# Kernel optimization log

Hardware: AMD Instinct MI355X
Metric: run time of the kernel (lower is better)

Reference implementation:

```python
import jax, jax.numpy as jnp
import numpy as np
from jax import lax

K = 64            # top-k channels kept per spatial location
GAMMA = 1.0       # noise scale (forward default)
NOISE_SCALE = 8.0 / 255.0


def setup_inputs() -> dict:
    key = jax.random.key(0)
    k1, k2, k3, k4 = jax.random.split(key, 4)
    B, Cin, Cout, H, W = 32, 128, 256, 64, 64
    x = jax.random.normal(k1, (B, Cin, H, W), dtype=jnp.float32)
    weight = jax.random.normal(k2, (Cout, Cin, 3, 3), dtype=jnp.float32) * 0.05
    relu_bias = jax.random.normal(k3, (Cout,), dtype=jnp.float32) * 0.1
    noise_u = jax.random.uniform(k4, (B, Cout, H, W), dtype=jnp.float32)
    return {"x": x, "weight": weight, "relu_bias": relu_bias, "noise_u": noise_u}


def reference(x, weight, relu_bias, noise_u):
    # conv3x3, stride 1, SAME padding, no bias (NCHW / OIHW)
    o = lax.conv_general_dilated(
        x, weight, window_strides=(1, 1), padding="SAME",
        dimension_numbers=("NCHW", "OIHW", "NCHW"))

    # per-output-channel bias = sum |W| over (in, kh, kw)  -> (1, Cout, 1, 1)
    bias = jnp.sum(jnp.abs(weight), axis=(1, 2, 3)).reshape(1, -1, 1, 1)

    # training-time uniform noise in [-gamma, gamma) scaled by bias*8/255
    o = o + bias * NOISE_SCALE * (noise_u * (2.0 * GAMMA) - GAMMA)

    # top-k masking over the channel dimension (per pixel)
    oc = jnp.moveaxis(o, 1, -1)                 # (B, H, W, C)
    topvals, _ = lax.top_k(oc, K)               # (B, H, W, K)
    thresh = topvals[..., K - 1:K]              # kth largest
    oc = jnp.where(oc >= thresh, oc, 0.0)
    o = jnp.moveaxis(oc, -1, 1)                 # back to (B, C, H, W)

    # trainable-bias ReLU: relu(o + b_c)
    o = jnp.maximum(o + relu_bias.reshape(1, -1, 1, 1), 0.0)
    return o
```

## Files before the change

kernel.cpp:

```cpp
#include <hip/hip_runtime.h>
#include <stdint.h>

#define BB 32
#define CIN 128
#define COUT 256
#define HH 64
#define WW 64
#define TOPK 64
#define NS_F (8.0f/255.0f)
#define GAPF 5e-4f
#define NS_D (8.0/255.0)
#define EPI_STRIDE 258
#define LIST_CAP 65536
#define XT_BYTES 33792

typedef __bf16 bf16x8 __attribute__((ext_vector_type(8)));
typedef float f32x4 __attribute__((ext_vector_type(4)));

__device__ __forceinline__ unsigned short bf_bits(float v) {
    __bf16 b = (__bf16)v;
    return __builtin_bit_cast(unsigned short, b);
}
__device__ __forceinline__ float bf_round(float v) { return (float)(__bf16)v; }

__device__ __forceinline__ int xoff(int ww, int s, int ci) {
    int byte = (ww << 9) + (s << 8) + (ci << 1);
    return byte ^ ((ww & 7) << 4);
}

__device__ __forceinline__ uint32_t skey32(float v) {
    uint32_t b = __float_as_uint(v);
    return (b & 0x80000000u) ? ~b : (b | 0x80000000u);
}
__device__ __forceinline__ float unskey32(uint32_t k) {
    uint32_t b = (k & 0x80000000u) ? (k & 0x7FFFFFFFu) : ~k;
    return __uint_as_float(b);
}

__device__ __forceinline__ uint64_t sortkey(double v) {
    uint64_t b = (uint64_t)__double_as_longlong(v);
    return (b & 0x8000000000000000ULL) ? ~b : (b | 0x8000000000000000ULL);
}
__device__ __forceinline__ double unsortkey(uint64_t k) {
    uint64_t b = (k & 0x8000000000000000ULL) ? (k & 0x7FFFFFFFFFFFFFFFULL) : ~k;
    return __longlong_as_double((long long)b);
}

__device__ __forceinline__ void select64_u32(const uint32_t u[4], uint32_t& k64, uint32_t& k65, int& bestcnt) {
    uint32_t prefix = 0;
    bestcnt = 256;
    for (int bit = 31; bit >= 0; --bit) {
        uint32_t cand = prefix | (1u << bit);
        int cnt = __popcll(__ballot(u[0] >= cand)) + __popcll(__ballot(u[1] >= cand))
                + __popcll(__ballot(u[2] >= cand)) + __popcll(__ballot(u[3] >= cand));
        if (cnt >= TOPK) {
            prefix = cand;
            bestcnt = cnt;
            if (cnt == TOPK) break;
        }
    }
    uint32_t mn = 0xFFFFFFFFu, mx = 0u;
#pragma unroll
    for (int j = 0; j < 4; ++j) {
        if (u[j] >= prefix) { if (u[j] < mn) mn = u[j]; }
        else                { if (u[j] > mx) mx = u[j]; }
    }
    for (int m = 1; m < 64; m <<= 1) {
        uint32_t a = (uint32_t)__shfl_xor((int)mn, m, 64);
        if (a < mn) mn = a;
        uint32_t b = (uint32_t)__shfl_xor((int)mx, m, 64);
        if (b > mx) mx = b;
    }
    k64 = mn; k65 = mx;
}

__device__ __forceinline__ void select64(const uint64_t u[4], uint64_t& k64, uint64_t& k65) {
    uint64_t prefix = 0;
    for (int bit = 63; bit >= 0; --bit) {
        uint64_t cand = prefix | (1ULL << bit);
        int cnt = __popcll(__ballot(u[0] >= cand)) + __popcll(__ballot(u[1] >= cand))
                + __popcll(__ballot(u[2] >= cand)) + __popcll(__ballot(u[3] >= cand));
        if (cnt >= TOPK) {
            prefix = cand;
            if (cnt == TOPK) break;
        }
    }
    uint64_t mn = ~0ULL, mx = 0ULL;
#pragma unroll
    for (int j = 0; j < 4; ++j) {
        if (u[j] >= prefix) { if (u[j] < mn) mn = u[j]; }
        else                { if (u[j] > mx) mx = u[j]; }
    }
    for (int m = 1; m < 64; m <<= 1) {
        uint64_t a = (uint64_t)__shfl_xor((unsigned long long)mn, m, 64);
        if (a < mn) mn = a;
        uint64_t b = (uint64_t)__shfl_xor((unsigned long long)mx, m, 64);
        if (b > mx) mx = b;
    }
    k64 = mn; k65 = mx;
}

__global__ __launch_bounds__(256) void prep_absw(const float* __restrict__ w,
                                                 double* __restrict__ absw,
                                                 int* __restrict__ counter) {
    const int c = blockIdx.x;
    const int t = threadIdx.x;
    if (c == 0 && t == 0) counter[0] = 0;
    double s = 0.0;
    for (int k = t; k < CIN * 9; k += 256) s += fabs((double)w[c * (CIN * 9) + k]);
    __shared__ double red[4];
    for (int m = 32; m; m >>= 1) s += __shfl_xor(s, m, 64);
    if ((t & 63) == 0) red[t >> 6] = s;
    __syncthreads();
    if (t == 0) absw[c] = red[0] + red[1] + red[2] + red[3];
}

__global__ __launch_bounds__(256) void prep_wT(const float* __restrict__ w,
                                               float* __restrict__ wT) {
    const int o0 = blockIdx.x * 16;
    const int c = threadIdx.x;
#pragma unroll
    for (int i = 0; i < 16; ++i) {
        int o = o0 + i;
        int r = o >> 7, ci = o & 127;
        wT[(size_t)o * COUT + c] = w[(size_t)(c * CIN + ci) * 9 + r];
    }
}

__global__ __launch_bounds__(128) void prep_wB(const float* __restrict__ w,
                                               unsigned short* __restrict__ wB) {
    const int c = blockIdx.x;
    const int ci = threadIdx.x;
#pragma unroll
    for (int r = 0; r < 9; ++r) {
        float v = w[((size_t)c * CIN + ci) * 9 + r];
        float hf = bf_round(v);
        wB[((size_t)r * COUT + c) * CIN + ci] = bf_bits(v);
        wB[((size_t)(9 + r) * COUT + c) * CIN + ci] = bf_bits(v - hf);
    }
}

__global__ __launch_bounds__(256, 2) void fused_kernel(
    const float* __restrict__ x,
    const float* __restrict__ relu_bias,
    const float* __restrict__ noise,
    const double* __restrict__ absw,
    const unsigned short* __restrict__ wB,
    float* __restrict__ out,
    int* __restrict__ counter,
    int* __restrict__ list) {

    __shared__ alignas(16) union {
        unsigned short xT[2 * 66 * 256];
        float o[32 * EPI_STRIDE];
    } U;
    __shared__ float lds_absw[COUT];
    __shared__ float lds_bias[COUT];
    __shared__ uint32_t thrk[32];

    const int tid = threadIdx.x;
    const int lane = tid & 63;
    const int wv = tid >> 6;

    const int bid = ((int)(blockIdx.x & 7) << 7) + ((int)blockIdx.x >> 3);
    const int b0 = (bid >> 6) * 2;
    const int h = bid & 63;

    lds_absw[tid] = (float)absw[tid];
    lds_bias[tid] = relu_bias[tid];

    const int kgrp8 = (lane >> 4) << 3;

    f32x4 acc[2][4][4];
#pragma unroll
    for (int g = 0; g < 2; ++g)
#pragma unroll
        for (int i = 0; i < 4; ++i)
#pragma unroll
            for (int j = 0; j < 4; ++j) {
                acc[g][i][j][0] = 0.f; acc[g][i][j][1] = 0.f;
                acc[g][i][j][2] = 0.f; acc[g][i][j][3] = 0.f;
            }

    char* xb = (char*)U.xT;

    if (tid < 128) {
        int img = tid >> 6;
        int t = tid & 63;
        int wwz = (t & 32) ? 65 : 0;
        int sz = (t >> 4) & 1;
        int c0z = (t & 15) << 3;
        bf16x8 z;
#pragma unroll
        for (int j = 0; j < 8; ++j) z[j] = (__bf16)0.f;
        *(bf16x8*)(xb + img * XT_BYTES + xoff(wwz, sz, c0z)) = z;
    }

    const int laneB = ((lane & 15) << 7) + ((lane >> 4) << 3) + (wv << 13);

    for (int kh = 0; kh < 3; ++kh) {
        const int r = h + kh - 1;
        if (r < 0 || r >= HH) continue;
        __syncthreads();
        {
            const int w = lane;
#pragma unroll
            for (int img = 0; img < 2; ++img) {
                const float* xr = x + (((size_t)(b0 + img) * CIN) * HH + (size_t)r) * WW;
                char* xbi = xb + img * XT_BYTES;
#pragma unroll
                for (int rep = 0; rep < 4; ++rep) {
                    const int c0 = rep * 32 + wv * 8;
                    const float* px = xr + (size_t)c0 * (HH * WW) + w;
                    bf16x8 hv, lv;
#pragma unroll
                    for (int j = 0; j < 8; ++j) {
                        float v = px[j * (HH * WW)];
                        float hf = bf_round(v);
                        hv[j] = (__bf16)v;
                        lv[j] = (__bf16)(v - hf);
                    }
                    *(bf16x8*)(xbi + xoff(w + 1, 0, c0)) = hv;
                    *(bf16x8*)(xbi + xoff(w + 1, 1, c0)) = lv;
                }
            }
        }
        __syncthreads();
#pragma unroll 1
        for (int ci0 = 0; ci0 < CIN; ci0 += 32) {
#pragma unroll
            for (int kw = 0; kw < 3; ++kw) {
                const unsigned short* wp0 = wB + (size_t)(kh * 3 + kw) * 32768 + ci0 + laneB;
                const unsigned short* wp1 = wp0 + (size_t)9 * 32768;
                bf16x8 bh[4], bl[4];
#pragma unroll
                for (int nt = 0; nt < 4; ++nt) {
                    bh[nt] = *(const bf16x8*)(wp0 + nt * 2048);
                    bl[nt] = *(const bf16x8*)(wp1 + nt * 2048);
                }
                bf16x8 ah[2][4], al[2][4];
#pragma unroll
                for (int img = 0; img < 2; ++img)
#pragma unroll
                    for (int mt = 0; mt < 4; ++mt) {
                        const int ww = (mt << 4) + (lane & 15) + kw;
                        ah[img][mt] = *(const bf16x8*)(xb + img * XT_BYTES + xoff(ww, 0, ci0 + kgrp8));
                        al[img][mt] = *(const bf16x8*)(xb + img * XT_BYTES + xoff(ww, 1, ci0 + kgrp8));
                    }
#pragma unroll
                for (int img = 0; img < 2; ++img)
#pragma unroll
                    for (int nt = 0; nt < 4; ++nt) {
#pragma unroll
                        for (int mt = 0; mt < 4; ++mt)
                            acc[img][mt][nt] = __builtin_amdgcn_mfma_f32_16x16x32_bf16(ah[img][mt], bh[nt], acc[img][mt][nt], 0, 0, 0);
#pragma unroll
                        for (int mt = 0; mt < 4; ++mt)
                            acc[img][mt][nt] = __builtin_amdgcn_mfma_f32_16x16x32_bf16(al[img][mt], bh[nt], acc[img][mt][nt], 0, 0, 0);
#pragma unroll
                        for (int mt = 0; mt < 4; ++mt)
                            acc[img][mt][nt] = __builtin_amdgcn_mfma_f32_16x16x32_bf16(ah[img][mt], bl[nt], acc[img][mt][nt], 0, 0, 0);
                    }
            }
        }
    }

#pragma unroll
    for (int img = 0; img < 2; ++img) {
        const int b = b0 + img;
#pragma unroll
        for (int q = 0; q < 2; ++q) {
            __syncthreads();
            {
                const int pl0 = (lane >> 4) << 2;
                const int cb = (wv << 6) + (lane & 15);
#pragma unroll
                for (int half = 0; half < 2; ++half) {
                    const int mt = q * 2 + half;
#pragma unroll
                    for (int nt = 0; nt < 4; ++nt)
#pragma unroll
                        for (int rr = 0; rr < 4; ++rr)
                            U.o[(half * 16 + pl0 + rr) * EPI_STRIDE + cb + nt * 16] = acc[img][mt][nt][rr];
                }
            }
            __syncthreads();
            {
                int wl = tid & 31;
                int cg = tid >> 5;
                int wg = q * 32 + wl;
#pragma unroll 4
                for (int it = 0; it < 32; ++it) {
                    int c = cg + 8 * it;
                    float u = noise[((size_t)(b * COUT + c) * HH + h) * WW + wg];
                    U.o[wl * EPI_STRIDE + c] += lds_absw[c] * NS_F * (2.f * u - 1.f);
                }
            }
            __syncthreads();
            {
#pragma unroll 1
                for (int pp = 0; pp < 8; ++pp) {
                    int pl = wv * 8 + pp;
                    uint32_t u[4];
#pragma unroll
                    for (int j = 0; j < 4; ++j)
                        u[j] = skey32(U.o[pl * EPI_STRIDE + lane + 64 * j]);
                    uint32_t k64, k65; int bcnt;
                    select64_u32(u, k64, k65, bcnt);
                    if (lane == 0) {
                        thrk[pl] = k64;
                        float t64 = unskey32(k64), t65 = unskey32(k65);
                        if (bcnt != 64 || t64 - t65 < GAPF) {
                            int idx = atomicAdd(counter, 1);
                            if (idx < LIST_CAP) list[idx] = (b << 12) | (h << 6) | (q * 32 + pl);
                        }
                    }
                }
            }
            __syncthreads();
            {
                int wl = tid & 31;
                int cg = tid >> 5;
                int wg = q * 32 + wl;
                uint32_t tk = thrk[wl];
#pragma unroll 4
                for (int it = 0; it < 32; ++it) {
                    int c = cg + 8 * it;
                    float v = U.o[wl * EPI_STRIDE + c];
                    float o = (skey32(v) >= tk ? v : 0.f) + lds_bias[c];
                    out[((size_t)(b * COUT + c) * HH + h) * WW + wg] = fmaxf(o, 0.f);
                }
            }
        }
    }
}

__global__ __launch_bounds__(256, 2) void fixup_kernel(
    const float* __restrict__ x,
    const float* __restrict__ wT,
    const float* __restrict__ relu_bias,
    const float* __restrict__ noise,
    const double* __restrict__ absw,
    float* __restrict__ out,
    const int* __restrict__ counter,
    const int* __restrict__ list) {

    __shared__ double xs[4][CIN * 9];
    __shared__ uint64_t keys[4][COUT];

    int n = counter[0];
    if (n > LIST_CAP) n = LIST_CAP;

    for (int base = blockIdx.x * 4; base < n; base += gridDim.x * 4) {
        const int np = min(4, n - base);
        __syncthreads();
        for (int q = 0; q < np; ++q) {
            int pix = list[base + q];
            int bb = pix >> 12, hh = (pix >> 6) & 63, ww = pix & 63;
            for (int t = threadIdx.x; t < CIN * 9; t += 256) {
                int r = t >> 7, ci = t & 127;
                int kh = r / 3, kw = r % 3;
                int hr = hh + kh - 1, wr = ww + kw - 1;
                xs[q][t] = (hr >= 0 && hr < HH && wr >= 0 && wr < WW)
                    ? (double)x[(((size_t)(bb * CIN + ci) * HH + hr) * WW) + wr] : 0.0;
            }
        }
        __syncthreads();
        const int c = threadIdx.x;
        double s[4] = {0.0, 0.0, 0.0, 0.0};
        for (int row = 0; row < CIN * 9; ++row) {
            double wv = (double)wT[(size_t)row * COUT + c];
            s[0] = fma(wv, xs[0][row], s[0]);
            s[1] = fma(wv, xs[1][row], s[1]);
            s[2] = fma(wv, xs[2][row], s[2]);
            s[3] = fma(wv, xs[3][row], s[3]);
        }
#pragma unroll 1
        for (int q = 0; q < np; ++q) {
            int pix = list[base + q];
            int bb = pix >> 12, hh = (pix >> 6) & 63, ww = pix & 63;
            double u = (double)noise[(((size_t)(bb * COUT + c) * HH + hh) * WW) + ww];
            s[q] += absw[c] * NS_D * (2.0 * u - 1.0);
            keys[q][c] = sortkey(s[q]);
        }
        __syncthreads();
#pragma unroll 1
        for (int q = 0; q < np; ++q) {
            uint64_t uu[4];
            int lane = threadIdx.x & 63;
#pragma unroll
            for (int j = 0; j < 4; ++j) uu[j] = keys[q][lane + 64 * j];
            uint64_t k64, k65;
            select64(uu, k64, k65);
            double t64 = unsortkey(k64);
            int pix = list[base + q];
            int bb = pix >> 12, hh = (pix >> 6) & 63, ww = pix & 63;
            double o = (s[q] >= t64 ? s[q] : 0.0) + (double)relu_bias[c];
            out[(((size_t)(bb * COUT + c) * HH + hh) * WW) + ww] = (float)fmax(o, 0.0);
        }
    }
}

extern "C" void kernel_launch(void* const* d_in, const int* in_sizes, int n_in,
                              void* d_out, int out_size, void* d_ws, size_t ws_size,
                              hipStream_t stream) {
    const float* x         = (const float*)d_in[0];
    const float* weight    = (const float*)d_in[1];
    const float* relu_bias = (const float*)d_in[2];
    const float* noise_u   = (const float*)d_in[3];
    float* out = (float*)d_out;

    char* ws = (char*)d_ws;
    double* absw          = (double*)ws;
    float*  wT            = (float*)(ws + 2048);
    int*    cnt           = (int*)(ws + 2048 + 1179648);
    int*    list          = (int*)(ws + 2048 + 1179648 + 16);
    unsigned short* wBq   = (unsigned short*)(ws + 2048 + 1179648 + 16 + 262144);

    prep_absw<<<COUT, 256, 0, stream>>>(weight, absw, cnt);
    prep_wT<<<72, 256, 0, stream>>>(weight, wT);
    prep_wB<<<COUT, 128, 0, stream>>>(weight, wBq);
    fused_kernel<<<(BB / 2) * HH, 256, 0, stream>>>(x, relu_bias, noise_u, absw, wBq, out, cnt, list);
    fixup_kernel<<<512, 256, 0, stream>>>(x, wT, relu_bias, noise_u, absw, out, cnt, list);
}
```

Baseline: 717.4 us.

## Fuse weight prep kernels, double-buffer B fragments, widen epilogue, tighten fixup gap

Merges the three weight-prep kernels into one launch. The MFMA inner loop now prefetches the next step's weight fragments into a ping-pong register set, processes the two images sequentially to cut A-fragment register pressure, and raises wave priority around the MFMA bursts. The epilogue handles all 64 pixels in a single pass using a larger LDS buffer with fewer barriers. The fixup gap threshold is halved so fewer pixels are sent to the exact fallback, and the fixup grid is doubled. The larger LDS union and the added prefetch registers may reduce occupancy, and the smaller gap depends on the precision margin of the split-bf16 product.

Result: faster. 696.6 us (-2.9%).

```diff
diff --git a/kernel.cpp b/kernel.cpp
--- a/kernel.cpp
+++ b/kernel.cpp
@@ -8,7 +8,7 @@
 #define WW 64
 #define TOPK 64
 #define NS_F (8.0f/255.0f)
-#define GAPF 5e-4f
+#define GAPF 2.5e-4f
 #define NS_D (8.0/255.0)
 #define EPI_STRIDE 258
 #define LIST_CAP 65536
@@ -100,45 +100,77 @@
     k64 = mn; k65 = mx;
 }
 
-__global__ __launch_bounds__(256) void prep_absw(const float* __restrict__ w,
-                                                 double* __restrict__ absw,
-                                                 int* __restrict__ counter) {
-    const int c = blockIdx.x;
-    const int t = threadIdx.x;
-    if (c == 0 && t == 0) counter[0] = 0;
-    double s = 0.0;
-    for (int k = t; k < CIN * 9; k += 256) s += fabs((double)w[c * (CIN * 9) + k]);
-    __shared__ double red[4];
-    for (int m = 32; m; m >>= 1) s += __shfl_xor(s, m, 64);
-    if ((t & 63) == 0) red[t >> 6] = s;
-    __syncthreads();
-    if (t == 0) absw[c] = red[0] + red[1] + red[2] + red[3];
-}
-
-__global__ __launch_bounds__(256) void prep_wT(const float* __restrict__ w,
-                                               float* __restrict__ wT) {
-    const int o0 = blockIdx.x * 16;
-    const int c = threadIdx.x;
-#pragma unroll
-    for (int i = 0; i < 16; ++i) {
-        int o = o0 + i;
-        int r = o >> 7, ci = o & 127;
-        wT[(size_t)o * COUT + c] = w[(size_t)(c * CIN + ci) * 9 + r];
-    }
-}
-
-__global__ __launch_bounds__(128) void prep_wB(const float* __restrict__ w,
-                                               unsigned short* __restrict__ wB) {
+__global__ __launch_bounds__(128) void prep_all(const float* __restrict__ w,
+                                                double* __restrict__ absw,
+                                                float* __restrict__ wT,
+                                                unsigned short* __restrict__ wB,
+                                                int* __restrict__ counter) {
     const int c = blockIdx.x;
     const int ci = threadIdx.x;
+    if (c == 0 && ci == 0) counter[0] = 0;
+    double s = 0.0;
 #pragma unroll
     for (int r = 0; r < 9; ++r) {
         float v = w[((size_t)c * CIN + ci) * 9 + r];
+        s += fabs((double)v);
         float hf = bf_round(v);
+        wT[((size_t)(r * CIN) + ci) * COUT + c] = v;
         wB[((size_t)r * COUT + c) * CIN + ci] = bf_bits(v);
         wB[((size_t)(9 + r) * COUT + c) * CIN + ci] = bf_bits(v - hf);
     }
-}
+    __shared__ double red[2];
+    for (int m = 32; m; m >>= 1) s += __shfl_xor(s, m, 64);
+    if ((ci & 63) == 0) red[ci >> 6] = s;
+    __syncthreads();
+    if (ci == 0) absw[c] = red[0] + red[1];
+}
+
+#define CONV_STEP(BH, BL, BHN, BLN, DO_PF)                                          \
+  {                                                                                 \
+    bf16x8 ah[4], al[4];                                                            \
+    _Pragma("unroll") for (int mt = 0; mt < 4; ++mt) {                              \
+      const int ww = (mt << 4) + (lane & 15) + kw;                                  \
+      ah[mt] = *(const bf16x8*)(xb + xoff(ww, 0, ci0 + kgrp8));                     \
+      al[mt] = *(const bf16x8*)(xb + xoff(ww, 1, ci0 + kgrp8));                     \
+    }                                                                               \
+    if (DO_PF) {                                                                    \
+      const int kwN = (kw == 2) ? 0 : kw + 1;                                       \
+      const int ciN = (kw == 2) ? ci0 + 32 : ci0;                                   \
+      const unsigned short* wpN0 = wB + (size_t)(kh * 3 + kwN) * 32768 + ciN + laneB; \
+      const unsigned short* wpN1 = wpN0 + (size_t)9 * 32768;                        \
+      _Pragma("unroll") for (int nt = 0; nt < 4; ++nt) {                            \
+        BHN[nt] = *(const bf16x8*)(wpN0 + nt * 2048);                               \
+        BLN[nt] = *(const bf16x8*)(wpN1 + nt * 2048);                               \
+      }                                                                             \
+    }                                                                               \
+    __builtin_amdgcn_s_setprio(1);                                                  \
+    _Pragma("unroll") for (int nt = 0; nt < 4; ++nt) {                              \
+      _Pragma("unroll") for (int mt = 0; mt < 4; ++mt)                              \
+        acc[0][mt][nt] = __builtin_amdgcn_mfma_f32_16x16x32_bf16(ah[mt], BH[nt], acc[0][mt][nt], 0, 0, 0); \
+      _Pragma("unroll") for (int mt = 0; mt < 4; ++mt)                              \
+        acc[0][mt][nt] = __builtin_amdgcn_mfma_f32_16x16x32_bf16(al[mt], BH[nt], acc[0][mt][nt], 0, 0, 0); \
+      _Pragma("unroll") for (int mt = 0; mt < 4; ++mt)                              \
+        acc[0][mt][nt] = __builtin_amdgcn_mfma_f32_16x16x32_bf16(ah[mt], BL[nt], acc[0][mt][nt], 0, 0, 0); \
+    }                                                                               \
+    __builtin_amdgcn_s_setprio(0);                                                  \
+    _Pragma("unroll") for (int mt = 0; mt < 4; ++mt) {                              \
+      const int ww = (mt << 4) + (lane & 15) + kw;                                  \
+      ah[mt] = *(const bf16x8*)(xb + XT_BYTES + xoff(ww, 0, ci0 + kgrp8));          \
+      al[mt] = *(const bf16x8*)(xb + XT_BYTES + xoff(ww, 1, ci0 + kgrp8));          \
+    }                                                                               \
+    __builtin_amdgcn_s_setprio(1);                                                  \
+    _Pragma("unroll") for (int nt = 0; nt < 4; ++nt) {                              \
+      _Pragma("unroll") for (int mt = 0; mt < 4; ++mt)                              \
+        acc[1][mt][nt] = __builtin_amdgcn_mfma_f32_16x16x32_bf16(ah[mt], BH[nt], acc[1][mt][nt], 0, 0, 0); \
+      _Pragma("unroll") for (int mt = 0; mt < 4; ++mt)                              \
+        acc[1][mt][nt] = __builtin_amdgcn_mfma_f32_16x16x32_bf16(al[mt], BH[nt], acc[1][mt][nt], 0, 0, 0); \
+      _Pragma("unroll") for (int mt = 0; mt < 4; ++mt)                              \
+        acc[1][mt][nt] = __builtin_amdgcn_mfma_f32_16x16x32_bf16(ah[mt], BL[nt], acc[1][mt][nt], 0, 0, 0); \
+    }                                                                               \
+    __builtin_amdgcn_s_setprio(0);                                                  \
+    kw = (kw == 2) ? 0 : kw + 1;                                                    \
+    if (kw == 0) ci0 += 32;                                                         \
+  }
 
 __global__ __launch_bounds__(256, 2) void fused_kernel(
     const float* __restrict__ x,
@@ -152,11 +184,11 @@
 
     __shared__ alignas(16) union {
         unsigned short xT[2 * 66 * 256];
-        float o[32 * EPI_STRIDE];
+        float o[64 * EPI_STRIDE];
     } U;
     __shared__ float lds_absw[COUT];
     __shared__ float lds_bias[COUT];
-    __shared__ uint32_t thrk[32];
+    __shared__ uint32_t thrk[64];
 
     const int tid = threadIdx.x;
     const int lane = tid & 63;
@@ -225,111 +257,85 @@
                 }
             }
         }
-        __syncthreads();
+        bf16x8 bhA[4], blA[4], bhB[4], blB[4];
+        {
+            const unsigned short* wpP0 = wB + (size_t)(kh * 3) * 32768 + laneB;
+            const unsigned short* wpP1 = wpP0 + (size_t)9 * 32768;
+#pragma unroll
+            for (int nt = 0; nt < 4; ++nt) {
+                bhA[nt] = *(const bf16x8*)(wpP0 + nt * 2048);
+                blA[nt] = *(const bf16x8*)(wpP1 + nt * 2048);
+            }
+        }
+        __syncthreads();
+        int ci0 = 0, kw = 0;
 #pragma unroll 1
-        for (int ci0 = 0; ci0 < CIN; ci0 += 32) {
-#pragma unroll
-            for (int kw = 0; kw < 3; ++kw) {
-                const unsigned short* wp0 = wB + (size_t)(kh * 3 + kw) * 32768 + ci0 + laneB;
-                const unsigned short* wp1 = wp0 + (size_t)9 * 32768;
-                bf16x8 bh[4], bl[4];
-#pragma unroll
-                for (int nt = 0; nt < 4; ++nt) {
-                    bh[nt] = *(const bf16x8*)(wp0 + nt * 2048);
-                    bl[nt] = *(const bf16x8*)(wp1 + nt * 2048);
-                }
-                bf16x8 ah[2][4], al[2][4];
-#pragma unroll
-                for (int img = 0; img < 2; ++img)
-#pragma unroll
-                    for (int mt = 0; mt < 4; ++mt) {
-                        const int ww = (mt << 4) + (lane & 15) + kw;
-                        ah[img][mt] = *(const bf16x8*)(xb + img * XT_BYTES + xoff(ww, 0, ci0 + kgrp8));
-                        al[img][mt] = *(const bf16x8*)(xb + img * XT_BYTES + xoff(ww, 1, ci0 + kgrp8));
-                    }
-#pragma unroll
-                for (int img = 0; img < 2; ++img)
-#pragma unroll
-                    for (int nt = 0; nt < 4; ++nt) {
-#pragma unroll
-                        for (int mt = 0; mt < 4; ++mt)
-                            acc[img][mt][nt] = __builtin_amdgcn_mfma_f32_16x16x32_bf16(ah[img][mt], bh[nt], acc[img][mt][nt], 0, 0, 0);
-#pragma unroll
-                        for (int mt = 0; mt < 4; ++mt)
-                            acc[img][mt][nt] = __builtin_amdgcn_mfma_f32_16x16x32_bf16(al[img][mt], bh[nt], acc[img][mt][nt], 0, 0, 0);
-#pragma unroll
-                        for (int mt = 0; mt < 4; ++mt)
-                            acc[img][mt][nt] = __builtin_amdgcn_mfma_f32_16x16x32_bf16(ah[img][mt], bl[nt], acc[img][mt][nt], 0, 0, 0);
-                    }
-            }
+        for (int it6 = 0; it6 < 6; ++it6) {
+            CONV_STEP(bhA, blA, bhB, blB, true);
+            CONV_STEP(bhB, blB, bhA, blA, (it6 < 5));
         }
     }
 
 #pragma unroll
     for (int img = 0; img < 2; ++img) {
         const int b = b0 + img;
-#pragma unroll
-        for (int q = 0; q < 2; ++q) {
-            __syncthreads();
-            {
-                const int pl0 = (lane >> 4) << 2;
-                const int cb = (wv << 6) + (lane & 15);
-#pragma unroll
-                for (int half = 0; half < 2; ++half) {
-                    const int mt = q * 2 + half;
-#pragma unroll
-                    for (int nt = 0; nt < 4; ++nt)
-#pragma unroll
-                        for (int rr = 0; rr < 4; ++rr)
-                            U.o[(half * 16 + pl0 + rr) * EPI_STRIDE + cb + nt * 16] = acc[img][mt][nt][rr];
-                }
-            }
-            __syncthreads();
-            {
-                int wl = tid & 31;
-                int cg = tid >> 5;
-                int wg = q * 32 + wl;
+        __syncthreads();
+        {
+            const int pl0 = (lane >> 4) << 2;
+            const int cb = (wv << 6) + (lane & 15);
+#pragma unroll
+            for (int mt = 0; mt < 4; ++mt)
+#pragma unroll
+                for (int nt = 0; nt < 4; ++nt)
+#pragma unroll
+                    for (int rr = 0; rr < 4; ++rr)
+                        U.o[(mt * 16 + pl0 + rr) * EPI_STRIDE + cb + nt * 16] = acc[img][mt][nt][rr];
+        }
+        __syncthreads();
+        {
+            int wl = tid & 63;
+            int cg = tid >> 6;
+            const float* np = noise + ((size_t)(b * COUT + cg) * HH + h) * WW + wl;
 #pragma unroll 4
-                for (int it = 0; it < 32; ++it) {
-                    int c = cg + 8 * it;
-                    float u = noise[((size_t)(b * COUT + c) * HH + h) * WW + wg];
-                    U.o[wl * EPI_STRIDE + c] += lds_absw[c] * NS_F * (2.f * u - 1.f);
-                }
-            }
-            __syncthreads();
-            {
+            for (int it = 0; it < 64; ++it) {
+                int c = cg + 4 * it;
+                float u = np[(size_t)(4 * it) * (HH * WW)];
+                U.o[wl * EPI_STRIDE + c] += lds_absw[c] * NS_F * (2.f * u - 1.f);
+            }
+        }
+        __syncthreads();
+        {
 #pragma unroll 1
-                for (int pp = 0; pp < 8; ++pp) {
-                    int pl = wv * 8 + pp;
-                    uint32_t u[4];
-#pragma unroll
-                    for (int j = 0; j < 4; ++j)
-                        u[j] = skey32(U.o[pl * EPI_STRIDE + lane + 64 * j]);
-                    uint32_t k64, k65; int bcnt;
-                    select64_u32(u, k64, k65, bcnt);
-                    if (lane == 0) {
-                        thrk[pl] = k64;
-                        float t64 = unskey32(k64), t65 = unskey32(k65);
-                        if (bcnt != 64 || t64 - t65 < GAPF) {
-                            int idx = atomicAdd(counter, 1);
-                            if (idx < LIST_CAP) list[idx] = (b << 12) | (h << 6) | (q * 32 + pl);
-                        }
+            for (int pp = 0; pp < 16; ++pp) {
+                int pl = wv * 16 + pp;
+                uint32_t u[4];
+#pragma unroll
+                for (int j = 0; j < 4; ++j)
+                    u[j] = skey32(U.o[pl * EPI_STRIDE + lane + 64 * j]);
+                uint32_t k64, k65; int bcnt;
+                select64_u32(u, k64, k65, bcnt);
+                if (lane == 0) {
+                    thrk[pl] = k64;
+                    float t64 = unskey32(k64), t65 = unskey32(k65);
+                    if (bcnt != 64 || t64 - t65 < GAPF) {
+                        int idx = atomicAdd(counter, 1);
+                        if (idx < LIST_CAP) list[idx] = (b << 12) | (h << 6) | pl;
                     }
                 }
             }
-            __syncthreads();
-            {
-                int wl = tid & 31;
-                int cg = tid >> 5;
-                int wg = q * 32 + wl;
-                uint32_t tk = thrk[wl];
+        }
+        __syncthreads();
+        {
+            int wl = tid & 63;
+            int cg = tid >> 6;
+            uint32_t tk = thrk[wl];
+            float* op = out + ((size_t)(b * COUT + cg) * HH + h) * WW + wl;
 #pragma unroll 4
-                for (int it = 0; it < 32; ++it) {
-                    int c = cg + 8 * it;
-                    float v = U.o[wl * EPI_STRIDE + c];
-                    float o = (skey32(v) >= tk ? v : 0.f) + lds_bias[c];
-                    out[((size_t)(b * COUT + c) * HH + h) * WW + wg] = fmaxf(o, 0.f);
-                }
+            for (int it = 0; it < 64; ++it) {
+                int c = cg + 4 * it;
+                float v = U.o[wl * EPI_STRIDE + c];
+                float o = (skey32(v) >= tk ? v : 0.f) + lds_bias[c];
+                op[(size_t)(4 * it) * (HH * WW)] = fmaxf(o, 0.f);
             }
         }
     }
@@ -417,9 +423,7 @@
     int*    list          = (int*)(ws + 2048 + 1179648 + 16);
     unsigned short* wBq   = (unsigned short*)(ws + 2048 + 1179648 + 16 + 262144);
 
-    prep_absw<<<COUT, 256, 0, stream>>>(weight, absw, cnt);
-    prep_wT<<<72, 256, 0, stream>>>(weight, wT);
-    prep_wB<<<COUT, 128, 0, stream>>>(weight, wBq);
+    prep_all<<<COUT, 128, 0, stream>>>(weight, absw, wT, wBq, cnt);
     fused_kernel<<<(BB / 2) * HH, 256, 0, stream>>>(x, relu_bias, noise_u, absw, wBq, out, cnt, list);
-    fixup_kernel<<<512, 256, 0, stream>>>(x, wT, relu_bias, noise_u, absw, out, cnt, list);
-}
+    fixup_kernel<<<1024, 256, 0, stream>>>(x, wT, relu_bias, noise_u, absw, out, cnt, list);
+}
```

## Merge weight prep kernels, halve gap threshold, widen fixup batching

Applied to the files above, without the earlier changes.

Replaces the three weight-preparation kernels with a single prep_all kernel that computes |W| sums, the transposed fp32 weights and the split-bf16 weights in one pass. This removes launches and repeated reads of the weights. The near-tie gap threshold for the fixup list is halved, so fewer pixels get flagged for exact recomputation. The fixup kernel now batches 8 pixels per block instead of 4, stores inputs in float shared memory and launches twice the grid. The tighter gap risks missing top-k boundary ties that the bf16 path gets wrong.

After: 805.8 us. 12.3% more time.

```diff
diff --git a/kernel.cpp b/kernel.cpp
--- a/kernel.cpp
+++ b/kernel.cpp
@@ -8,7 +8,7 @@
 #define WW 64
 #define TOPK 64
 #define NS_F (8.0f/255.0f)
-#define GAPF 5e-4f
+#define GAPF 2.5e-4f
 #define NS_D (8.0/255.0)
 #define EPI_STRIDE 258
 #define LIST_CAP 65536
@@ -100,44 +100,29 @@
     k64 = mn; k65 = mx;
 }
 
-__global__ __launch_bounds__(256) void prep_absw(const float* __restrict__ w,
-                                                 double* __restrict__ absw,
-                                                 int* __restrict__ counter) {
-    const int c = blockIdx.x;
-    const int t = threadIdx.x;
-    if (c == 0 && t == 0) counter[0] = 0;
-    double s = 0.0;
-    for (int k = t; k < CIN * 9; k += 256) s += fabs((double)w[c * (CIN * 9) + k]);
-    __shared__ double red[4];
-    for (int m = 32; m; m >>= 1) s += __shfl_xor(s, m, 64);
-    if ((t & 63) == 0) red[t >> 6] = s;
-    __syncthreads();
-    if (t == 0) absw[c] = red[0] + red[1] + red[2] + red[3];
-}
-
-__global__ __launch_bounds__(256) void prep_wT(const float* __restrict__ w,
-                                               float* __restrict__ wT) {
-    const int o0 = blockIdx.x * 16;
-    const int c = threadIdx.x;
-#pragma unroll
-    for (int i = 0; i < 16; ++i) {
-        int o = o0 + i;
-        int r = o >> 7, ci = o & 127;
-        wT[(size_t)o * COUT + c] = w[(size_t)(c * CIN + ci) * 9 + r];
-    }
-}
-
-__global__ __launch_bounds__(128) void prep_wB(const float* __restrict__ w,
-                                               unsigned short* __restrict__ wB) {
+__global__ __launch_bounds__(128) void prep_all(const float* __restrict__ w,
+                                                double* __restrict__ absw,
+                                                float* __restrict__ wT,
+                                                unsigned short* __restrict__ wB,
+                                                int* __restrict__ counter) {
     const int c = blockIdx.x;
     const int ci = threadIdx.x;
+    if (c == 0 && ci == 0) counter[0] = 0;
+    double s = 0.0;
 #pragma unroll
     for (int r = 0; r < 9; ++r) {
         float v = w[((size_t)c * CIN + ci) * 9 + r];
+        s += fabs((double)v);
         float hf = bf_round(v);
+        wT[((size_t)(r * CIN) + ci) * COUT + c] = v;
         wB[((size_t)r * COUT + c) * CIN + ci] = bf_bits(v);
         wB[((size_t)(9 + r) * COUT + c) * CIN + ci] = bf_bits(v - hf);
     }
+    __shared__ double red[2];
+    for (int m = 32; m; m >>= 1) s += __shfl_xor(s, m, 64);
+    if ((ci & 63) == 0) red[ci >> 6] = s;
+    __syncthreads();
+    if (ci == 0) absw[c] = red[0] + red[1];
 }
 
 __global__ __launch_bounds__(256, 2) void fused_kernel(
@@ -345,14 +330,14 @@
     const int* __restrict__ counter,
     const int* __restrict__ list) {
 
-    __shared__ double xs[4][CIN * 9];
-    __shared__ uint64_t keys[4][COUT];
+    __shared__ float xs[8][CIN * 9];
+    __shared__ uint64_t keys[8][COUT];
 
     int n = counter[0];
     if (n > LIST_CAP) n = LIST_CAP;
 
-    for (int base = blockIdx.x * 4; base < n; base += gridDim.x * 4) {
-        const int np = min(4, n - base);
+    for (int base = blockIdx.x * 8; base < n; base += gridDim.x * 8) {
+        const int np = min(8, n - base);
         __syncthreads();
         for (int q = 0; q < np; ++q) {
             int pix = list[base + q];
@@ -362,18 +347,18 @@
                 int kh = r / 3, kw = r % 3;
                 int hr = hh + kh - 1, wr = ww + kw - 1;
                 xs[q][t] = (hr >= 0 && hr < HH && wr >= 0 && wr < WW)
-                    ? (double)x[(((size_t)(bb * CIN + ci) * HH + hr) * WW) + wr] : 0.0;
+                    ? x[(((size_t)(bb * CIN + ci) * HH + hr) * WW) + wr] : 0.0f;
             }
         }
         __syncthreads();
         const int c = threadIdx.x;
-        double s[4] = {0.0, 0.0, 0.0, 0.0};
+        double s[8] = {0.0, 0.0, 0.0, 0.0, 0.0, 0.0, 0.0, 0.0};
+#pragma unroll 2
         for (int row = 0; row < CIN * 9; ++row) {
             double wv = (double)wT[(size_t)row * COUT + c];
-            s[0] = fma(wv, xs[0][row], s[0]);
-            s[1] = fma(wv, xs[1][row], s[1]);
-            s[2] = fma(wv, xs[2][row], s[2]);
-            s[3] = fma(wv, xs[3][row], s[3]);
+#pragma unroll
+            for (int q = 0; q < 8; ++q)
+                s[q] = fma(wv, (double)xs[q][row], s[q]);
         }
 #pragma unroll 1
         for (int q = 0; q < np; ++q) {
@@ -417,9 +402,7 @@
     int*    list          = (int*)(ws + 2048 + 1179648 + 16);
     unsigned short* wBq   = (unsigned short*)(ws + 2048 + 1179648 + 16 + 262144);
 
-    prep_absw<<<COUT, 256, 0, stream>>>(weight, absw, cnt);
-    prep_wT<<<72, 256, 0, stream>>>(weight, wT);
-    prep_wB<<<COUT, 128, 0, stream>>>(weight, wBq);
+    prep_all<<<COUT, 128, 0, stream>>>(weight, absw, wT, wBq, cnt);
     fused_kernel<<<(BB / 2) * HH, 256, 0, stream>>>(x, relu_bias, noise_u, absw, wBq, out, cnt, list);
-    fixup_kernel<<<512, 256, 0, stream>>>(x, wT, relu_bias, noise_u, absw, out, cnt, list);
-}
+    fixup_kernel<<<1024, 256, 0, stream>>>(x, wT, relu_bias, noise_u, absw, out, cnt, list);
+}
```
